# Performance work log

Hardware: AMD Instinct MI355X
Metric: run time of the kernel (lower is better)

## Reference

```python
import jax, jax.numpy as jnp
import numpy as np

B, S, HID = 2, 2048, 2048
NH, DN, DR, DV, RANK = 16, 128, 64, 128, 512
DQK = DN + DR
SCALE = DQK ** -0.5
EPS = 1e-5


def _rope(x, theta):
    # x: [..., d] with d even; theta broadcastable to [..., d//2] (angle per pair)
    x1, x2 = x[..., 0::2], x[..., 1::2]
    c, s = jnp.cos(theta), jnp.sin(theta)
    return jnp.stack([x1 * c - x2 * s, x1 * s + x2 * c], axis=-1).reshape(x.shape)


def _layernorm(x, gamma, beta):
    mu = jnp.mean(x, axis=-1, keepdims=True)
    var = jnp.var(x, axis=-1, keepdims=True)
    return (x - mu) * jax.lax.rsqrt(var + EPS) * gamma + beta


def setup_inputs() -> dict:
    key = jax.random.key(0)
    ks = jax.random.split(key, 8)
    def xavier(k, fan_in, fan_out, gain=1.0):
        lim = gain * np.sqrt(6.0 / (fan_in + fan_out))
        return jax.random.uniform(k, (fan_in, fan_out), jnp.float32, -lim, lim)
    return {
        "hidden_states": jax.random.normal(ks[0], (B, S, HID), jnp.float32),
        "freqs_cis": jax.random.uniform(ks[1], (S, DR // 2), jnp.float32) * 2.0 * np.pi,
        "Wq": xavier(ks[2], HID, NH * DQK),                      # q_proj (stored [in,out])
        "Wkv_a": xavier(ks[3], HID, RANK + DR),                  # kv_proj_a
        "kv_gamma": jnp.ones((RANK,), jnp.float32),              # kv_norm
        "kv_beta": jnp.zeros((RANK,), jnp.float32),
        "Wkv_b": xavier(ks[4], RANK, NH * (DN + DV)),            # kv_proj_b
        "Wout": xavier(ks[5], NH * DV, HID, gain=1.0 / np.sqrt(2.0)),  # out_proj
    }


def reference(hidden_states, freqs_cis, Wq, Wkv_a, kv_gamma, kv_beta, Wkv_b, Wout):
    b, s, _ = hidden_states.shape
    max_len = freqs_cis.shape[0]
    pos = jnp.arange(s) % max_len                      # [s], position_ids=None path
    theta = freqs_cis[pos]                             # [s, DR//2]

    # Q projection, split nope/rope, partial RoPE
    q = (hidden_states @ Wq).reshape(b, s, NH, DQK)
    q_nope, q_rope = q[..., :DN], q[..., DN:]
    q_rope = _rope(q_rope, theta[None, :, None, :])    # [b,s,nh,DR]

    # Low-rank KV: compressed latent + shared rope key
    kv = hidden_states @ Wkv_a                         # [b,s,RANK+DR]
    kv_c, k_rope = kv[..., :RANK], kv[..., RANK:]
    k_rope = _rope(k_rope, theta[None, :, :])          # [b,s,DR]
    kv_c = _layernorm(kv_c, kv_gamma, kv_beta)
    kvb = (kv_c @ Wkv_b).reshape(b, s, NH, DN + DV)
    k_nope, v = kvb[..., :DN], kvb[..., DN:]
    k = jnp.concatenate(
        [k_nope, jnp.broadcast_to(k_rope[:, :, None, :], (b, s, NH, DR))], axis=-1)

    q = jnp.concatenate([q_nope, q_rope], axis=-1)     # [b,s,nh,DQK]
    scores = jnp.einsum('bthd,bshd->btsh', q, k) * SCALE
    weights = jax.nn.softmax(scores.astype(jnp.float32), axis=2).astype(q.dtype)
    attn = jnp.einsum('btsh,bshd->bthd', weights, v).reshape(b, s, NH * DV)
    return attn @ Wout
```

## Files before the change

kernel.cpp:

```cpp
#include <hip/hip_runtime.h>

#define BATCH 2
#define SEQ   2048
#define HID   2048
#define NH    16
#define DN    128
#define DR    64
#define DV    128
#define RANK  512
#define DQK   192
#define NQ    (NH*DQK)
#define NQKV  3840
#define NKVB  (NH*(DN+DV))
#define NTOK  (BATCH*SEQ)
#define SCALE_F 0.07216878364870323f
#define SCALE_LOG2E 0.10411754831420211f

typedef __bf16 bf16x8 __attribute__((ext_vector_type(8)));
typedef float  f32x4  __attribute__((ext_vector_type(4)));
typedef unsigned int u32x4 __attribute__((ext_vector_type(4)));
typedef unsigned short u16;
typedef unsigned short u16x4 __attribute__((ext_vector_type(4)));

__device__ __forceinline__ float b2f(u16 h) {
    unsigned int u = ((unsigned int)h) << 16;
    float f; __builtin_memcpy(&f, &u, 4); return f;
}
__device__ __forceinline__ u16 f2b(float f) {
    unsigned int x; __builtin_memcpy(&x, &f, 4);
    unsigned int r = x + 0x7fffu + ((x >> 16) & 1u);
    return (u16)(r >> 16);
}
__device__ __forceinline__ bf16x8 lds_frag(const u16* p) {
    u32x4 v = *(const u32x4*)p;
    return __builtin_bit_cast(bf16x8, v);
}
__device__ __forceinline__ bf16x8 to_frag(u32x4 v) {
    return __builtin_bit_cast(bf16x8, v);
}
__device__ __forceinline__ f32x4 mfma16(bf16x8 a, bf16x8 b, f32x4 c) {
    return __builtin_amdgcn_mfma_f32_16x16x32_bf16(a, b, c, 0, 0, 0);
}
__device__ __forceinline__ void store_out(u16* p, float v) { *p = f2b(v); }
__device__ __forceinline__ void store_out(float* p, float v) { *p = v; }
__device__ __forceinline__ void gld_lds16(const u16* g, u16* l) {
    __builtin_amdgcn_global_load_lds(
        (const __attribute__((address_space(1))) unsigned int*)g,
        (__attribute__((address_space(3))) unsigned int*)l, 16, 0, 0);
}

__global__ __launch_bounds__(256) void prep_kernel(
        const float* __restrict__ hs_f, u16* __restrict__ hs,
        const float* __restrict__ Wq, const float* __restrict__ Wkva,
        const float* __restrict__ Wkvb, const float* __restrict__ Wout,
        u16* __restrict__ WqkvT, u16* __restrict__ WkvbT, u16* __restrict__ WoutT) {
    int tid = threadIdx.x;
    int bid = blockIdx.x;
    if (bid < 8192) {
        int i = bid * 256 + tid;
        f32x4 v = *(const f32x4*)(hs_f + (size_t)i * 4);
        u16 o[4];
        for (int k = 0; k < 4; k++) o[k] = f2b(v[k]);
        *(unsigned long long*)(hs + (size_t)i * 4) = *(unsigned long long*)o;
        return;
    }
    bid -= 8192;
    const float* in; u16* out; int R, C, tilesC;
    if (bid < 1536)      { in = Wq;   out = WqkvT;                       R = HID;  C = NQ;   tilesC = 48; }
    else if (bid < 1920) { bid -= 1536; in = Wkva; out = WqkvT + (size_t)NQ * HID; R = HID; C = 576; tilesC = 12; }
    else if (bid < 2432) { bid -= 1920; in = Wkvb; out = WkvbT;          R = RANK; C = NKVB; tilesC = 64; }
    else                 { bid -= 2432; in = Wout; out = WoutT;          R = HID;  C = HID;  tilesC = 32; }
    __shared__ unsigned int t32[64 * 65];
    int r0 = (bid / tilesC) * 64, c0 = (bid % tilesC) * 64;
    bool valid = (c0 < C);
    for (int i = 0; i < 4; i++) {
        int u = tid + i * 256;
        int rl = u >> 4, c4 = u & 15;
        f32x4 v = {0.f, 0.f, 0.f, 0.f};
        if (valid) v = *(const f32x4*)&in[(size_t)(r0 + rl) * C + c0 + c4 * 4];
        for (int j = 0; j < 4; j++)
            t32[(c4 * 4 + j) * 65 + rl] = f2b(v[j]);
    }
    __syncthreads();
    for (int i = 0; i < 2; i++) {
        int u = tid + i * 256;
        int cl = u >> 3, r8 = (u & 7) * 8;
        unsigned int w[8];
        for (int j = 0; j < 8; j++) w[j] = t32[cl * 65 + r8 + j];
        u32x4 pk;
        for (int j = 0; j < 4; j++) pk[j] = (w[2 * j] & 0xffffu) | (w[2 * j + 1] << 16);
        *(u32x4*)&out[(size_t)(c0 + cl) * R + r0 + r8] = pk;
    }
}

template <typename OutT>
__global__ __launch_bounds__(256) void gemm_bt(const u16* __restrict__ A,
                                               const u16* __restrict__ Bt,
                                               OutT* __restrict__ C,
                                               int K, int lda, int ldb, int ldc) {
    __shared__ u16 As[128 * 32];
    __shared__ u16 Bs[128 * 32];
    int tid = threadIdx.x, lane = tid & 63, w = tid >> 6;
    int wm = (w >> 1) * 64, wn = (w & 1) * 64;
    int g = lane >> 4, ln = lane & 15;
    int m0 = blockIdx.y * 128, n0 = blockIdx.x * 128;
    f32x4 acc[4][4] = {};
    for (int k0 = 0; k0 < K; k0 += 32) {
        for (int i = 0; i < 2; i++) {
            int ch = tid + i * 256;
            int row = ch >> 2, o = ch & 3;
            gld_lds16(&A[(size_t)(m0 + row) * lda + k0 + o * 8], &As[row * 32 + o * 8]);
            gld_lds16(&Bt[(size_t)(n0 + row) * ldb + k0 + o * 8], &Bs[row * 32 + o * 8]);
        }
        __syncthreads();
        bf16x8 af[4], bf[4];
        for (int i = 0; i < 4; i++) af[i] = lds_frag(&As[(wm + i * 16 + ln) * 32 + g * 8]);
        for (int j = 0; j < 4; j++) bf[j] = lds_frag(&Bs[(wn + j * 16 + ln) * 32 + g * 8]);
        for (int i = 0; i < 4; i++)
            for (int j = 0; j < 4; j++)
                acc[i][j] = mfma16(af[i], bf[j], acc[i][j]);
        __syncthreads();
    }
    for (int i = 0; i < 4; i++)
        for (int j = 0; j < 4; j++)
            for (int r = 0; r < 4; r++) {
                int m = m0 + wm + i * 16 + g * 4 + r;
                int n = n0 + wn + j * 16 + ln;
                store_out(&C[(size_t)m * ldc + n], acc[i][j][r]);
            }
}

template <typename OutT>
__global__ __launch_bounds__(512, 2) void gemm256(const u16* __restrict__ A,
                                                  const u16* __restrict__ Bt,
                                                  OutT* __restrict__ C,
                                                  int K, int lda, int ldb, int ldc) {
    __shared__ u16 lds[8][128 * 64];
    int tid = threadIdx.x, lane = tid & 63, w = tid >> 6;
    int wm = w >> 2, wn = w & 3;
    int g = lane >> 4, ln = lane & 15;
    int m0 = blockIdx.y * 256, n0 = blockIdx.x * 256;

    int srow = tid >> 3, schunk = tid & 7;
    int cs = schunk ^ (srow & 7);
    int sdst = tid * 8;

    auto stage = [&](int p, int ht, int t) {
        const u16* src = (ht < 2) ? A : Bt;
        int ld = (ht < 2) ? lda : ldb;
        int base = ((ht < 2) ? m0 : n0) + (ht & 1) * 128;
        u16* buf = lds[p * 4 + ht];
        int k0 = t << 6;
        gld_lds16(&src[(size_t)(base + srow) * ld + k0 + cs * 8], &buf[sdst]);
        gld_lds16(&src[(size_t)(base + 64 + srow) * ld + k0 + cs * 8], &buf[4096 + sdst]);
    };

    int aR = ln * 64;
    int ck0 = ((g ^ (ln & 7)) << 3);
    int ck1 = (((4 + g) ^ (ln & 7)) << 3);
    int bB = (wn & 1) * 4096;

    f32x4 acc[8][4] = {};
    int NT = K >> 6;

    for (int ht = 0; ht < 4; ht++) stage(0, ht, 0);
    __builtin_amdgcn_sched_barrier(0);
    asm volatile("s_waitcnt vmcnt(0)" ::: "memory");
    __builtin_amdgcn_sched_barrier(0);
    __builtin_amdgcn_s_barrier();

    for (int t = 0; t < NT; t++) {
        const u16* Ab = lds[(t & 1) * 4 + wm];
        const u16* Bb = lds[(t & 1) * 4 + 2 + (wn >> 1)];
        int pn = (t & 1) ^ 1;
        bool pf = (t + 1 < NT);
        bf16x8 af[4][2], bf[4][2];

#pragma unroll
        for (int f = 0; f < 4; f++) {
            af[f][0] = lds_frag(&Ab[f * 1024 + aR + ck0]);
            af[f][1] = lds_frag(&Ab[f * 1024 + aR + ck1]);
        }
#pragma unroll
        for (int nf = 0; nf < 2; nf++) {
            bf[nf][0] = lds_frag(&Bb[bB + nf * 1024 + aR + ck0]);
            bf[nf][1] = lds_frag(&Bb[bB + nf * 1024 + aR + ck1]);
        }
        if (pf) { stage(pn, 0, t + 1); stage(pn, 1, t + 1); }
        __builtin_amdgcn_s_barrier();
        __builtin_amdgcn_s_setprio(1);
#pragma unroll
        for (int f = 0; f < 4; f++)
#pragma unroll
            for (int nf = 0; nf < 2; nf++) {
                acc[f][nf] = mfma16(af[f][0], bf[nf][0], acc[f][nf]);
                acc[f][nf] = mfma16(af[f][1], bf[nf][1], acc[f][nf]);
            }
        __builtin_amdgcn_s_setprio(0);

#pragma unroll
        for (int nf = 2; nf < 4; nf++) {
            bf[nf][0] = lds_frag(&Bb[bB + nf * 1024 + aR + ck0]);
            bf[nf][1] = lds_frag(&Bb[bB + nf * 1024 + aR + ck1]);
        }
        if (pf) { stage(pn, 2, t + 1); stage(pn, 3, t + 1); }
        __builtin_amdgcn_s_barrier();
        __builtin_amdgcn_s_setprio(1);
#pragma unroll
        for (int f = 0; f < 4; f++)
#pragma unroll
            for (int nf = 2; nf < 4; nf++) {
                acc[f][nf] = mfma16(af[f][0], bf[nf][0], acc[f][nf]);
                acc[f][nf] = mfma16(af[f][1], bf[nf][1], acc[f][nf]);
            }
        __builtin_amdgcn_s_setprio(0);

#pragma unroll
        for (int f = 0; f < 4; f++) {
            af[f][0] = lds_frag(&Ab[(f + 4) * 1024 + aR + ck0]);
            af[f][1] = lds_frag(&Ab[(f + 4) * 1024 + aR + ck1]);
        }
        __builtin_amdgcn_s_barrier();
        __builtin_amdgcn_s_setprio(1);
#pragma unroll
        for (int f = 0; f < 4; f++)
#pragma unroll
            for (int nf = 0; nf < 2; nf++) {
                acc[f + 4][nf] = mfma16(af[f][0], bf[nf][0], acc[f + 4][nf]);
                acc[f + 4][nf] = mfma16(af[f][1], bf[nf][1], acc[f + 4][nf]);
            }
        __builtin_amdgcn_s_setprio(0);

        __builtin_amdgcn_s_barrier();
        __builtin_amdgcn_s_setprio(1);
#pragma unroll
        for (int f = 0; f < 4; f++)
#pragma unroll
            for (int nf = 2; nf < 4; nf++) {
                acc[f + 4][nf] = mfma16(af[f][0], bf[nf][0], acc[f + 4][nf]);
                acc[f + 4][nf] = mfma16(af[f][1], bf[nf][1], acc[f + 4][nf]);
            }
        __builtin_amdgcn_s_setprio(0);

        if (pf) {
            __builtin_amdgcn_sched_barrier(0);
            asm volatile("s_waitcnt vmcnt(0)" ::: "memory");
            __builtin_amdgcn_sched_barrier(0);
            __builtin_amdgcn_s_barrier();
        }
    }

#pragma unroll
    for (int f = 0; f < 8; f++)
#pragma unroll
        for (int nf = 0; nf < 4; nf++)
#pragma unroll
            for (int r = 0; r < 4; r++) {
                int m = m0 + wm * 128 + f * 16 + g * 4 + r;
                int n = n0 + wn * 64 + nf * 16 + ln;
                store_out(&C[(size_t)m * ldc + n], acc[f][nf][r]);
            }
}

__global__ void rope_q(u16* __restrict__ qkv, const float* __restrict__ freqs) {
    int token = blockIdx.x;
    int s = token & (SEQ - 1);
    int tid = threadIdx.x;
    for (int i = 0; i < 2; i++) {
        int idx = tid + i * 256;
        int hh = idx >> 5, p = idx & 31;
        float th = freqs[s * 32 + p];
        float c = __cosf(th), sn = __sinf(th);
        size_t off = (size_t)token * NQKV + hh * DQK + DN + 2 * p;
        float x1 = b2f(qkv[off]), x2 = b2f(qkv[off + 1]);
        qkv[off]     = f2b(x1 * c - x2 * sn);
        qkv[off + 1] = f2b(x1 * sn + x2 * c);
    }
}

__global__ void ln_kv(const u16* __restrict__ qkv, const float* __restrict__ gamma,
                      const float* __restrict__ beta, u16* __restrict__ kv_c) {
    int row = blockIdx.x, tid = threadIdx.x;
    size_t base = (size_t)row * NQKV + NQ;
    float x0 = b2f(qkv[base + tid]), x1 = b2f(qkv[base + 256 + tid]);
    float s = x0 + x1, q2 = x0 * x0 + x1 * x1;
    for (int o = 32; o > 0; o >>= 1) { s += __shfl_xor(s, o); q2 += __shfl_xor(q2, o); }
    __shared__ float sh[8];
    int lane = tid & 63, w = tid >> 6;
    if (lane == 0) { sh[w] = s; sh[4 + w] = q2; }
    __syncthreads();
    float S = sh[0] + sh[1] + sh[2] + sh[3];
    float Q2 = sh[4] + sh[5] + sh[6] + sh[7];
    float mu = S * (1.f / 512.f);
    float var = Q2 * (1.f / 512.f) - mu * mu;
    float rs = rsqrtf(var + 1e-5f);
    kv_c[(size_t)row * RANK + tid] =
        f2b((x0 - mu) * rs * gamma[tid] + beta[tid]);
    kv_c[(size_t)row * RANK + 256 + tid] =
        f2b((x1 - mu) * rs * gamma[256 + tid] + beta[256 + tid]);
}

__global__ void k_assemble(const u16* __restrict__ kvb, const u16* __restrict__ qkv,
                           const float* __restrict__ freqs, u16* __restrict__ Kf) {
    int token = blockIdx.x;
    int b = token >> 11;
    int s = token & (SEQ - 1);
    int tid = threadIdx.x;
    __shared__ u16 roped[64];
    if (tid < 32) {
        int p = tid;
        float th = freqs[s * 32 + p];
        float c = __cosf(th), sn = __sinf(th);
        float x1 = b2f(qkv[(size_t)token * NQKV + NQ + RANK + 2 * p]);
        float x2 = b2f(qkv[(size_t)token * NQKV + NQ + RANK + 2 * p + 1]);
        roped[2 * p]     = f2b(x1 * c - x2 * sn);
        roped[2 * p + 1] = f2b(x1 * sn + x2 * c);
    }
    __syncthreads();
    int kt = s >> 6, r = s & 63;
    int swr = ((r >> 1) & 3) * 8;
    {
        int hh = tid >> 4, c8 = (tid & 15) * 8;
        size_t dst = ((size_t)(b * NH + hh) * 32 + kt) * 12288
                   + (size_t)(c8 >> 5) * 2048 + r * 32 + ((c8 & 31) ^ swr);
        *(u32x4*)&Kf[dst] = *(const u32x4*)&kvb[(size_t)token * NKVB + hh * 256 + c8];
    }
    if (tid < 128) {
        int hh = tid >> 3, c8 = (tid & 7) * 8;
        size_t dst = ((size_t)(b * NH + hh) * 32 + kt) * 12288
                   + (size_t)(4 + (c8 >> 5)) * 2048 + r * 32 + ((c8 & 31) ^ swr);
        *(u32x4*)&Kf[dst] = *(u32x4*)&roped[c8];
    }
}

__global__ void v_transpose(const u16* __restrict__ kvb, u16* __restrict__ Vt) {
    __shared__ unsigned int t32[64 * 65];
    int bx = blockIdx.x;
    int st = bx * 64, dt = blockIdx.y * 64;
    int b = blockIdx.z >> 4, h = blockIdx.z & 15;
    int tid = threadIdx.x;
    for (int i = 0; i < 2; i++) {
        int u = tid + i * 256;
        int sl = u >> 3, c8 = (u & 7) * 8;
        u32x4 v = *(const u32x4*)&kvb[((size_t)(b * SEQ + st + sl) * NH + h) * 256 + DN + dt + c8];
        for (int j = 0; j < 4; j++) {
            t32[(c8 + 2 * j) * 65 + sl]     = v[j] & 0xffffu;
            t32[(c8 + 2 * j + 1) * 65 + sl] = v[j] >> 16;
        }
    }
    __syncthreads();
    for (int i = 0; i < 2; i++) {
        int u = tid + i * 256;
        int dl = u >> 3, s8 = (u & 7) * 8;
        unsigned int w[8];
        for (int j = 0; j < 8; j++) w[j] = t32[dl * 65 + s8 + j];
        u32x4 pk;
        for (int j = 0; j < 4; j++) pk[j] = (w[2 * j] & 0xffffu) | (w[2 * j + 1] << 16);
        size_t dst = ((size_t)(b * NH + h) * 32 + bx) * 8192
                   + (size_t)(s8 >> 5) * 4096 + (size_t)(dt + dl) * 32 + (s8 & 31);
        *(u32x4*)&Vt[dst] = pk;
    }
}

#define KC    64
#define QTILE 64
#define NIT  (SEQ / KC)
__global__ __launch_bounds__(256, 4) void attn_kernel(const u16* __restrict__ Q,
                                                      const u16* __restrict__ Kf,
                                                      const u16* __restrict__ Vt,
                                                      u16* __restrict__ O) {
    __shared__ u16 Ks[6 * 64 * 32];
    __shared__ u16 Ps[2][QTILE * 64];
    int tid = threadIdx.x, lane = tid & 63, w = tid >> 6;
    int w1 = w & 1;
    int w2 = w >> 1;
    int g = lane >> 4, ln = lane & 15;
    int bid = blockIdx.x;
    int swz = ((bid & 7) << 7) | (bid >> 3);
    int qt = swz & 31, h = (swz >> 5) & 15, b = swz >> 9;

    size_t qbase = ((size_t)(b * SEQ + qt * QTILE)) * NQKV + h * DQK;
    const u16* Kh = Kf + (size_t)(b * NH + h) * (32 * 12288);
    const u16* Vh = Vt + (size_t)(b * NH + h) * (32 * 8192);

    u32x4 qreg[2][6];
#pragma unroll
    for (int ni = 0; ni < 2; ni++)
#pragma unroll
        for (int kk = 0; kk < 6; kk++) {
            const u16* qp = &Q[qbase + (size_t)(w1 * 32 + ni * 16 + ln) * NQKV + kk * 32 + g * 8];
            asm volatile("global_load_dwordx4 %0, %1, off"
                         : "=v"(qreg[ni][kk]) : "v"(qp));
        }
#pragma unroll
    for (int i = 0; i < 6; i++)
        gld_lds16(&Kh[i * 2048 + tid * 8], &Ks[i * 2048 + tid * 8]);

    int kRd0 = (w2 * 32 + ln) * 64 + ((g * 16) ^ (((ln >> 1) & 3) << 4));
    int kRd1 = kRd0 + 16 * 64;
    int vrow = w2 * 2048 + ln * 32 + g * 8;
    int pswz = (ln & 7) << 4;

    f32x4 oacc[2][4] = {};
    float lpriv[2] = {0.f, 0.f};

    for (int kt = 0; kt < NIT; kt++) {
        asm volatile("s_waitcnt vmcnt(0)" ::: "memory");
        __builtin_amdgcn_sched_barrier(0);
        __syncthreads();
        const char* KsB = (const char*)Ks;
        f32x4 sacc[2][2] = {};
#pragma unroll
        for (int kk = 0; kk < 6; kk++) {
            bf16x8 af0 = lds_frag((const u16*)(KsB + kk * 4096 + kRd0));
            bf16x8 af1 = lds_frag((const u16*)(KsB + kk * 4096 + kRd1));
            bf16x8 q0 = to_frag(qreg[0][kk]), q1 = to_frag(qreg[1][kk]);
            sacc[0][0] = mfma16(af0, q0, sacc[0][0]);
            sacc[0][1] = mfma16(af0, q1, sacc[0][1]);
            sacc[1][0] = mfma16(af1, q0, sacc[1][0]);
            sacc[1][1] = mfma16(af1, q1, sacc[1][1]);
        }
        char* Pb = (char*)Ps[kt & 1];
#pragma unroll
        for (int mi = 0; mi < 2; mi++)
#pragma unroll
            for (int ni = 0; ni < 2; ni++) {
                float p0 = exp2f(sacc[mi][ni][0] * SCALE_LOG2E);
                float p1 = exp2f(sacc[mi][ni][1] * SCALE_LOG2E);
                float p2 = exp2f(sacc[mi][ni][2] * SCALE_LOG2E);
                float p3 = exp2f(sacc[mi][ni][3] * SCALE_LOG2E);
                lpriv[ni] += (p0 + p1) + (p2 + p3);
                unsigned int c0, c1;
                asm("v_cvt_pk_bf16_f32 %0, %1, %2" : "=v"(c0) : "v"(p0), "v"(p1));
                asm("v_cvt_pk_bf16_f32 %0, %1, %2" : "=v"(c1) : "v"(p2), "v"(p3));
                uint2 pk; pk.x = c0; pk.y = c1;
                int pwB = (w1 * 32 + ni * 16 + ln) * 128
                        + ((w2 * 64 + mi * 32 + g * 8) ^ pswz);
                *(uint2*)(Pb + pwB) = pk;
            }
        __syncthreads();
        if (kt + 1 < NIT) {
            const u16* kT = Kh + (size_t)(kt + 1) * 12288;
#pragma unroll
            for (int i = 0; i < 6; i++)
                gld_lds16(&kT[i * 2048 + tid * 8], &Ks[i * 2048 + tid * 8]);
        }
        const u16* vT = Vh + (size_t)kt * 8192;
#pragma unroll
        for (int kk = 0; kk < 2; kk++) {
            bf16x8 pa[2], vb[4];
#pragma unroll
            for (int mi = 0; mi < 2; mi++)
                pa[mi] = lds_frag((const u16*)(Pb + (w1 * 32 + mi * 16 + ln) * 128
                                               + ((kk * 64 + g * 16) ^ pswz)));
#pragma unroll
            for (int ni = 0; ni < 4; ni++)
                vb[ni] = to_frag(*(const u32x4*)&vT[kk * 4096 + ni * 512 + vrow]);
#pragma unroll
            for (int mi = 0; mi < 2; mi++)
#pragma unroll
                for (int ni = 0; ni < 4; ni++)
                    oacc[mi][ni] = mfma16(pa[mi], vb[ni], oacc[mi][ni]);
        }
    }

    float* lsumF = (float*)Ps[0];
    for (int ni = 0; ni < 2; ni++) {
        float v = lpriv[ni];
        v += __shfl_xor(v, 16);
        v += __shfl_xor(v, 32);
        if (g == 0) lsumF[w2 * 64 + w1 * 32 + ni * 16 + ln] = v;
    }
    __syncthreads();
    for (int mi = 0; mi < 2; mi++)
        for (int ni = 0; ni < 4; ni++) {
            int d = w2 * 64 + ni * 16 + ln;
            for (int r = 0; r < 4; r++) {
                int row = w1 * 32 + mi * 16 + g * 4 + r;
                float l = lsumF[row] + lsumF[64 + row];
                O[((size_t)(b * SEQ + qt * QTILE + row) * NH + h) * DV + d] =
                    f2b(oacc[mi][ni][r] / l);
            }
        }
}

extern "C" void kernel_launch(void* const* d_in, const int* in_sizes, int n_in,
                              void* d_out, int out_size, void* d_ws, size_t ws_size,
                              hipStream_t stream) {
    const float* hs_f  = (const float*)d_in[0];
    const float* freqs = (const float*)d_in[1];
    const float* Wq    = (const float*)d_in[2];
    const float* Wkva  = (const float*)d_in[3];
    const float* gamma = (const float*)d_in[4];
    const float* beta  = (const float*)d_in[5];
    const float* Wkvb  = (const float*)d_in[6];
    const float* Wout  = (const float*)d_in[7];
    float* outp = (float*)d_out;

    char* ws = (char*)d_ws;
    size_t off = 0;
    auto alloc = [&](size_t elems) -> u16* {
        u16* p = (u16*)(ws + off);
        off += ((elems * 2 + 255) / 256) * 256;
        return p;
    };
    u16* hs     = alloc((size_t)NTOK * HID);
    u16* WqkvT  = alloc((size_t)NQKV * HID);
    u16* WkvbT  = alloc((size_t)NKVB * RANK);
    u16* WoutT  = alloc((size_t)HID * HID);
    u16* qkv    = alloc((size_t)NTOK * NQKV);
    u16* kv_c   = alloc((size_t)NTOK * RANK);
    u16* kvb    = alloc((size_t)NTOK * NKVB);
    u16* Kf     = alloc((size_t)NTOK * NQ);
    u16* Vt     = alloc((size_t)BATCH * NH * DV * SEQ);
    u16* attn   = alloc((size_t)NTOK * NH * DV);
    (void)ws_size; (void)in_sizes; (void)n_in; (void)out_size;

    prep_kernel<<<8192 + 1536 + 384 + 512 + 1024, 256, 0, stream>>>(
        hs_f, hs, Wq, Wkva, Wkvb, Wout, WqkvT, WkvbT, WoutT);

    gemm256<<<dim3(NQKV / 256, NTOK / 256), 512, 0, stream>>>(hs, WqkvT, qkv, HID, HID, HID, NQKV);

    rope_q<<<NTOK, 256, 0, stream>>>(qkv, freqs);

    ln_kv<<<NTOK, 256, 0, stream>>>(qkv, gamma, beta, kv_c);

    gemm256<<<dim3(NKVB / 256, NTOK / 256), 512, 0, stream>>>(kv_c, WkvbT, kvb, RANK, RANK, RANK, NKVB);

    k_assemble<<<NTOK, 256, 0, stream>>>(kvb, qkv, freqs, Kf);

    v_transpose<<<dim3(SEQ / 64, DV / 64, BATCH * NH), 256, 0, stream>>>(kvb, Vt);

    attn_kernel<<<1024, 256, 0, stream>>>(qkv, Kf, Vt, attn);

    gemm_bt<<<dim3(HID / 128, NTOK / 128), 256, 0, stream>>>(attn, WoutT, outp, HID, HID, HID, HID);
}
```

Baseline: 421.9 us.

## Template big GEMM on M tile for out-proj; prefetch V into registers in attention

The pipelined 256-wide GEMM kernel is generalised with a BM template parameter so the output projection uses a 128x256 tile variant instead of the simple 128x128 single-buffered gemm_bt. In the attention kernel, V fragments are loaded into registers at the start of each key chunk so they overlap with the QK^T MFMAs. The P buffer is made single, barriers become explicit s_barrier with targeted waitcnts, and occupancy is lowered from 4 to 3 blocks. The register prefetch raises VGPR pressure, and single-buffering P depends on the added barriers for correctness.

```diff
diff --git a/kernel.cpp b/kernel.cpp
--- a/kernel.cpp
+++ b/kernel.cpp
@@ -93,63 +93,28 @@
     }
 }
 
-template <typename OutT>
-__global__ __launch_bounds__(256) void gemm_bt(const u16* __restrict__ A,
-                                               const u16* __restrict__ Bt,
-                                               OutT* __restrict__ C,
-                                               int K, int lda, int ldb, int ldc) {
-    __shared__ u16 As[128 * 32];
-    __shared__ u16 Bs[128 * 32];
-    int tid = threadIdx.x, lane = tid & 63, w = tid >> 6;
-    int wm = (w >> 1) * 64, wn = (w & 1) * 64;
-    int g = lane >> 4, ln = lane & 15;
-    int m0 = blockIdx.y * 128, n0 = blockIdx.x * 128;
-    f32x4 acc[4][4] = {};
-    for (int k0 = 0; k0 < K; k0 += 32) {
-        for (int i = 0; i < 2; i++) {
-            int ch = tid + i * 256;
-            int row = ch >> 2, o = ch & 3;
-            gld_lds16(&A[(size_t)(m0 + row) * lda + k0 + o * 8], &As[row * 32 + o * 8]);
-            gld_lds16(&Bt[(size_t)(n0 + row) * ldb + k0 + o * 8], &Bs[row * 32 + o * 8]);
-        }
-        __syncthreads();
-        bf16x8 af[4], bf[4];
-        for (int i = 0; i < 4; i++) af[i] = lds_frag(&As[(wm + i * 16 + ln) * 32 + g * 8]);
-        for (int j = 0; j < 4; j++) bf[j] = lds_frag(&Bs[(wn + j * 16 + ln) * 32 + g * 8]);
-        for (int i = 0; i < 4; i++)
-            for (int j = 0; j < 4; j++)
-                acc[i][j] = mfma16(af[i], bf[j], acc[i][j]);
-        __syncthreads();
-    }
-    for (int i = 0; i < 4; i++)
-        for (int j = 0; j < 4; j++)
-            for (int r = 0; r < 4; r++) {
-                int m = m0 + wm + i * 16 + g * 4 + r;
-                int n = n0 + wn + j * 16 + ln;
-                store_out(&C[(size_t)m * ldc + n], acc[i][j][r]);
-            }
-}
-
-template <typename OutT>
-__global__ __launch_bounds__(512, 2) void gemm256(const u16* __restrict__ A,
-                                                  const u16* __restrict__ Bt,
-                                                  OutT* __restrict__ C,
-                                                  int K, int lda, int ldb, int ldc) {
-    __shared__ u16 lds[8][128 * 64];
+template <int BM, typename OutT>
+__global__ __launch_bounds__(512, 2) void gemm256k(const u16* __restrict__ A,
+                                                   const u16* __restrict__ Bt,
+                                                   OutT* __restrict__ C,
+                                                   int K, int lda, int ldb, int ldc) {
+    constexpr int MH = BM / 128;
+    constexpr int NHALF = MH + 2;
+    __shared__ u16 lds[2 * NHALF][128 * 64];
     int tid = threadIdx.x, lane = tid & 63, w = tid >> 6;
     int wm = w >> 2, wn = w & 3;
     int g = lane >> 4, ln = lane & 15;
-    int m0 = blockIdx.y * 256, n0 = blockIdx.x * 256;
+    int m0 = blockIdx.y * BM, n0 = blockIdx.x * 256;
 
     int srow = tid >> 3, schunk = tid & 7;
     int cs = schunk ^ (srow & 7);
     int sdst = tid * 8;
 
     auto stage = [&](int p, int ht, int t) {
-        const u16* src = (ht < 2) ? A : Bt;
-        int ld = (ht < 2) ? lda : ldb;
-        int base = ((ht < 2) ? m0 : n0) + (ht & 1) * 128;
-        u16* buf = lds[p * 4 + ht];
+        const u16* src = (ht < MH) ? A : Bt;
+        int ld = (ht < MH) ? lda : ldb;
+        int base = (ht < MH) ? (m0 + ht * 128) : (n0 + (ht - MH) * 128);
+        u16* buf = lds[p * NHALF + ht];
         int k0 = t << 6;
         gld_lds16(&src[(size_t)(base + srow) * ld + k0 + cs * 8], &buf[sdst]);
         gld_lds16(&src[(size_t)(base + 64 + srow) * ld + k0 + cs * 8], &buf[4096 + sdst]);
@@ -159,27 +124,28 @@
     int ck0 = ((g ^ (ln & 7)) << 3);
     int ck1 = (((4 + g) ^ (ln & 7)) << 3);
     int bB = (wn & 1) * 4096;
-
-    f32x4 acc[8][4] = {};
+    int aBase = (BM == 256) ? 0 : wm * 4096;
+
+    f32x4 acc[MH * 4][4] = {};
     int NT = K >> 6;
 
-    for (int ht = 0; ht < 4; ht++) stage(0, ht, 0);
+    for (int ht = 0; ht < NHALF; ht++) stage(0, ht, 0);
     __builtin_amdgcn_sched_barrier(0);
     asm volatile("s_waitcnt vmcnt(0)" ::: "memory");
     __builtin_amdgcn_sched_barrier(0);
     __builtin_amdgcn_s_barrier();
 
     for (int t = 0; t < NT; t++) {
-        const u16* Ab = lds[(t & 1) * 4 + wm];
-        const u16* Bb = lds[(t & 1) * 4 + 2 + (wn >> 1)];
+        const u16* Ab = lds[(t & 1) * NHALF + ((BM == 256) ? wm : 0)];
+        const u16* Bb = lds[(t & 1) * NHALF + MH + (wn >> 1)];
         int pn = (t & 1) ^ 1;
         bool pf = (t + 1 < NT);
         bf16x8 af[4][2], bf[4][2];
 
 #pragma unroll
         for (int f = 0; f < 4; f++) {
-            af[f][0] = lds_frag(&Ab[f * 1024 + aR + ck0]);
-            af[f][1] = lds_frag(&Ab[f * 1024 + aR + ck1]);
+            af[f][0] = lds_frag(&Ab[aBase + f * 1024 + aR + ck0]);
+            af[f][1] = lds_frag(&Ab[aBase + f * 1024 + aR + ck1]);
         }
 #pragma unroll
         for (int nf = 0; nf < 2; nf++) {
@@ -203,7 +169,7 @@
             bf[nf][0] = lds_frag(&Bb[bB + nf * 1024 + aR + ck0]);
             bf[nf][1] = lds_frag(&Bb[bB + nf * 1024 + aR + ck1]);
         }
-        if (pf) { stage(pn, 2, t + 1); stage(pn, 3, t + 1); }
+        if (pf) { for (int ht = 2; ht < NHALF; ht++) stage(pn, ht, t + 1); }
         __builtin_amdgcn_s_barrier();
         __builtin_amdgcn_s_setprio(1);
 #pragma unroll
@@ -215,32 +181,34 @@
             }
         __builtin_amdgcn_s_setprio(0);
 
-#pragma unroll
-        for (int f = 0; f < 4; f++) {
-            af[f][0] = lds_frag(&Ab[(f + 4) * 1024 + aR + ck0]);
-            af[f][1] = lds_frag(&Ab[(f + 4) * 1024 + aR + ck1]);
-        }
-        __builtin_amdgcn_s_barrier();
-        __builtin_amdgcn_s_setprio(1);
-#pragma unroll
-        for (int f = 0; f < 4; f++)
-#pragma unroll
-            for (int nf = 0; nf < 2; nf++) {
-                acc[f + 4][nf] = mfma16(af[f][0], bf[nf][0], acc[f + 4][nf]);
-                acc[f + 4][nf] = mfma16(af[f][1], bf[nf][1], acc[f + 4][nf]);
+        if constexpr (BM == 256) {
+#pragma unroll
+            for (int f = 0; f < 4; f++) {
+                af[f][0] = lds_frag(&Ab[(f + 4) * 1024 + aR + ck0]);
+                af[f][1] = lds_frag(&Ab[(f + 4) * 1024 + aR + ck1]);
             }
-        __builtin_amdgcn_s_setprio(0);
-
-        __builtin_amdgcn_s_barrier();
-        __builtin_amdgcn_s_setprio(1);
-#pragma unroll
-        for (int f = 0; f < 4; f++)
-#pragma unroll
-            for (int nf = 2; nf < 4; nf++) {
-                acc[f + 4][nf] = mfma16(af[f][0], bf[nf][0], acc[f + 4][nf]);
-                acc[f + 4][nf] = mfma16(af[f][1], bf[nf][1], acc[f + 4][nf]);
-            }
-        __builtin_amdgcn_s_setprio(0);
+            __builtin_amdgcn_s_barrier();
+            __builtin_amdgcn_s_setprio(1);
+#pragma unroll
+            for (int f = 0; f < 4; f++)
+#pragma unroll
+                for (int nf = 0; nf < 2; nf++) {
+                    acc[f + 4][nf] = mfma16(af[f][0], bf[nf][0], acc[f + 4][nf]);
+                    acc[f + 4][nf] = mfma16(af[f][1], bf[nf][1], acc[f + 4][nf]);
+                }
+            __builtin_amdgcn_s_setprio(0);
+
+            __builtin_amdgcn_s_barrier();
+            __builtin_amdgcn_s_setprio(1);
+#pragma unroll
+            for (int f = 0; f < 4; f++)
+#pragma unroll
+                for (int nf = 2; nf < 4; nf++) {
+                    acc[f + 4][nf] = mfma16(af[f][0], bf[nf][0], acc[f + 4][nf]);
+                    acc[f + 4][nf] = mfma16(af[f][1], bf[nf][1], acc[f + 4][nf]);
+                }
+            __builtin_amdgcn_s_setprio(0);
+        }
 
         if (pf) {
             __builtin_amdgcn_sched_barrier(0);
@@ -251,12 +219,12 @@
     }
 
 #pragma unroll
-    for (int f = 0; f < 8; f++)
+    for (int f = 0; f < MH * 4; f++)
 #pragma unroll
         for (int nf = 0; nf < 4; nf++)
 #pragma unroll
             for (int r = 0; r < 4; r++) {
-                int m = m0 + wm * 128 + f * 16 + g * 4 + r;
+                int m = m0 + ((BM == 256) ? wm * 128 : wm * 64) + f * 16 + g * 4 + r;
                 int n = n0 + wn * 64 + nf * 16 + ln;
                 store_out(&C[(size_t)m * ldc + n], acc[f][nf][r]);
             }
@@ -365,12 +333,13 @@
 #define KC    64
 #define QTILE 64
 #define NIT  (SEQ / KC)
-__global__ __launch_bounds__(256, 4) void attn_kernel(const u16* __restrict__ Q,
+__global__ __launch_bounds__(256, 3) void attn_kernel(const u16* __restrict__ Q,
                                                       const u16* __restrict__ Kf,
                                                       const u16* __restrict__ Vt,
                                                       u16* __restrict__ O) {
     __shared__ u16 Ks[6 * 64 * 32];
-    __shared__ u16 Ps[2][QTILE * 64];
+    __shared__ u16 Ps[QTILE * 64];
+    __shared__ float lsumLDS[2][QTILE];
     int tid = threadIdx.x, lane = tid & 63, w = tid >> 6;
     int w1 = w & 1;
     int w2 = w >> 1;
@@ -392,13 +361,16 @@
             asm volatile("global_load_dwordx4 %0, %1, off"
                          : "=v"(qreg[ni][kk]) : "v"(qp));
         }
+    const u16* kTn = Kh;
 #pragma unroll
     for (int i = 0; i < 6; i++)
-        gld_lds16(&Kh[i * 2048 + tid * 8], &Ks[i * 2048 + tid * 8]);
+        gld_lds16(&kTn[i * 2048 + tid * 8], &Ks[i * 2048 + tid * 8]);
 
     int kRd0 = (w2 * 32 + ln) * 64 + ((g * 16) ^ (((ln >> 1) & 3) << 4));
     int kRd1 = kRd0 + 16 * 64;
     int vrow = w2 * 2048 + ln * 32 + g * 8;
+    const u16* vpA = Vh + vrow;
+    const u16* vpB = vpA + 4096;
     int pswz = (ln & 7) << 4;
 
     f32x4 oacc[2][4] = {};
@@ -407,7 +379,16 @@
     for (int kt = 0; kt < NIT; kt++) {
         asm volatile("s_waitcnt vmcnt(0)" ::: "memory");
         __builtin_amdgcn_sched_barrier(0);
-        __syncthreads();
+        __builtin_amdgcn_s_barrier();
+        u32x4 v00, v01, v02, v03, v10, v11, v12, v13;
+        asm volatile("global_load_dwordx4 %0, %1, off"             : "=v"(v00) : "v"(vpA));
+        asm volatile("global_load_dwordx4 %0, %1, off offset:1024" : "=v"(v01) : "v"(vpA));
+        asm volatile("global_load_dwordx4 %0, %1, off offset:2048" : "=v"(v02) : "v"(vpA));
+        asm volatile("global_load_dwordx4 %0, %1, off offset:3072" : "=v"(v03) : "v"(vpA));
+        asm volatile("global_load_dwordx4 %0, %1, off"             : "=v"(v10) : "v"(vpB));
+        asm volatile("global_load_dwordx4 %0, %1, off offset:1024" : "=v"(v11) : "v"(vpB));
+        asm volatile("global_load_dwordx4 %0, %1, off offset:2048" : "=v"(v12) : "v"(vpB));
+        asm volatile("global_load_dwordx4 %0, %1, off offset:3072" : "=v"(v13) : "v"(vpB));
         const char* KsB = (const char*)Ks;
         f32x4 sacc[2][2] = {};
 #pragma unroll
@@ -420,7 +401,7 @@
             sacc[1][0] = mfma16(af1, q0, sacc[1][0]);
             sacc[1][1] = mfma16(af1, q1, sacc[1][1]);
         }
-        char* Pb = (char*)Ps[kt & 1];
+        char* Pb = (char*)Ps;
 #pragma unroll
         for (int mi = 0; mi < 2; mi++)
 #pragma unroll
@@ -438,38 +419,49 @@
                         + ((w2 * 64 + mi * 32 + g * 8) ^ pswz);
                 *(uint2*)(Pb + pwB) = pk;
             }
-        __syncthreads();
+        asm volatile("s_waitcnt lgkmcnt(0)" ::: "memory");
+        __builtin_amdgcn_sched_barrier(0);
+        __builtin_amdgcn_s_barrier();
         if (kt + 1 < NIT) {
-            const u16* kT = Kh + (size_t)(kt + 1) * 12288;
+            kTn += 12288;
 #pragma unroll
             for (int i = 0; i < 6; i++)
-                gld_lds16(&kT[i * 2048 + tid * 8], &Ks[i * 2048 + tid * 8]);
-        }
-        const u16* vT = Vh + (size_t)kt * 8192;
-#pragma unroll
-        for (int kk = 0; kk < 2; kk++) {
-            bf16x8 pa[2], vb[4];
-#pragma unroll
-            for (int mi = 0; mi < 2; mi++)
-                pa[mi] = lds_frag((const u16*)(Pb + (w1 * 32 + mi * 16 + ln) * 128
-                                               + ((kk * 64 + g * 16) ^ pswz)));
-#pragma unroll
-            for (int ni = 0; ni < 4; ni++)
-                vb[ni] = to_frag(*(const u32x4*)&vT[kk * 4096 + ni * 512 + vrow]);
-#pragma unroll
-            for (int mi = 0; mi < 2; mi++)
-#pragma unroll
-                for (int ni = 0; ni < 4; ni++)
-                    oacc[mi][ni] = mfma16(pa[mi], vb[ni], oacc[mi][ni]);
-        }
-    }
-
-    float* lsumF = (float*)Ps[0];
+                gld_lds16(&kTn[i * 2048 + tid * 8], &Ks[i * 2048 + tid * 8]);
+            asm volatile("s_waitcnt vmcnt(6)" ::: "memory");
+        } else {
+            asm volatile("s_waitcnt vmcnt(0)" ::: "memory");
+        }
+        __builtin_amdgcn_sched_barrier(0);
+        {
+            bf16x8 pa0k0 = lds_frag((const u16*)(Pb + (w1 * 32 + ln) * 128 + ((g * 16) ^ pswz)));
+            bf16x8 pa1k0 = lds_frag((const u16*)(Pb + (w1 * 32 + 16 + ln) * 128 + ((g * 16) ^ pswz)));
+            bf16x8 pa0k1 = lds_frag((const u16*)(Pb + (w1 * 32 + ln) * 128 + ((64 + g * 16) ^ pswz)));
+            bf16x8 pa1k1 = lds_frag((const u16*)(Pb + (w1 * 32 + 16 + ln) * 128 + ((64 + g * 16) ^ pswz)));
+            oacc[0][0] = mfma16(pa0k0, to_frag(v00), oacc[0][0]);
+            oacc[0][1] = mfma16(pa0k0, to_frag(v01), oacc[0][1]);
+            oacc[0][2] = mfma16(pa0k0, to_frag(v02), oacc[0][2]);
+            oacc[0][3] = mfma16(pa0k0, to_frag(v03), oacc[0][3]);
+            oacc[1][0] = mfma16(pa1k0, to_frag(v00), oacc[1][0]);
+            oacc[1][1] = mfma16(pa1k0, to_frag(v01), oacc[1][1]);
+            oacc[1][2] = mfma16(pa1k0, to_frag(v02), oacc[1][2]);
+            oacc[1][3] = mfma16(pa1k0, to_frag(v03), oacc[1][3]);
+            oacc[0][0] = mfma16(pa0k1, to_frag(v10), oacc[0][0]);
+            oacc[0][1] = mfma16(pa0k1, to_frag(v11), oacc[0][1]);
+            oacc[0][2] = mfma16(pa0k1, to_frag(v12), oacc[0][2]);
+            oacc[0][3] = mfma16(pa0k1, to_frag(v13), oacc[0][3]);
+            oacc[1][0] = mfma16(pa1k1, to_frag(v10), oacc[1][0]);
+            oacc[1][1] = mfma16(pa1k1, to_frag(v11), oacc[1][1]);
+            oacc[1][2] = mfma16(pa1k1, to_frag(v12), oacc[1][2]);
+            oacc[1][3] = mfma16(pa1k1, to_frag(v13), oacc[1][3]);
+        }
+        vpA += 8192; vpB += 8192;
+    }
+
     for (int ni = 0; ni < 2; ni++) {
         float v = lpriv[ni];
         v += __shfl_xor(v, 16);
         v += __shfl_xor(v, 32);
-        if (g == 0) lsumF[w2 * 64 + w1 * 32 + ni * 16 + ln] = v;
+        if (g == 0) lsumLDS[w2][w1 * 32 + ni * 16 + ln] = v;
     }
     __syncthreads();
     for (int mi = 0; mi < 2; mi++)
@@ -477,7 +469,7 @@
             int d = w2 * 64 + ni * 16 + ln;
             for (int r = 0; r < 4; r++) {
                 int row = w1 * 32 + mi * 16 + g * 4 + r;
-                float l = lsumF[row] + lsumF[64 + row];
+                float l = lsumLDS[0][row] + lsumLDS[1][row];
                 O[((size_t)(b * SEQ + qt * QTILE + row) * NH + h) * DV + d] =
                     f2b(oacc[mi][ni][r] / l);
             }
@@ -519,13 +511,13 @@
     prep_kernel<<<8192 + 1536 + 384 + 512 + 1024, 256, 0, stream>>>(
         hs_f, hs, Wq, Wkva, Wkvb, Wout, WqkvT, WkvbT, WoutT);
 
-    gemm256<<<dim3(NQKV / 256, NTOK / 256), 512, 0, stream>>>(hs, WqkvT, qkv, HID, HID, HID, NQKV);
+    gemm256k<256><<<dim3(NQKV / 256, NTOK / 256), 512, 0, stream>>>(hs, WqkvT, qkv, HID, HID, HID, NQKV);
 
     rope_q<<<NTOK, 256, 0, stream>>>(qkv, freqs);
 
     ln_kv<<<NTOK, 256, 0, stream>>>(qkv, gamma, beta, kv_c);
 
-    gemm256<<<dim3(NKVB / 256, NTOK / 256), 512, 0, stream>>>(kv_c, WkvbT, kvb, RANK, RANK, RANK, NKVB);
+    gemm256k<256><<<dim3(NKVB / 256, NTOK / 256), 512, 0, stream>>>(kv_c, WkvbT, kvb, RANK, RANK, RANK, NKVB);
 
     k_assemble<<<NTOK, 256, 0, stream>>>(kvb, qkv, freqs, Kf);
 
@@ -533,5 +525,5 @@
 
     attn_kernel<<<1024, 256, 0, stream>>>(qkv, Kf, Vt, attn);
 
-    gemm_bt<<<dim3(HID / 128, NTOK / 128), 256, 0, stream>>>(attn, WoutT, outp, HID, HID, HID, HID);
-}
+    gemm256k<128><<<dim3(HID / 256, NTOK / 128), 512, 0, stream>>>(attn, WoutT, outp, HID, HID, HID, HID);
+}
```

Measured after the change: 420.0 us. About the same (-0.4%).
